# Kernel optimization log

Measured on AMD Instinct MI355X. Metric: run time of the kernel, lower is better.

## Reference

```python
import jax, jax.numpy as jnp
import numpy as np

G = 4      # deformable groups
K = 9      # 3x3 kernel points
EPS = 1e-5


def _bilinear_gather(value, loc_y, loc_x):
    # value: (N,H,W,G,Cg); loc_*: (N,H,W,G,K) float pixel coords, zero padding outside.
    N, H, W, g, Cg = value.shape
    y0f = jnp.floor(loc_y); x0f = jnp.floor(loc_x)
    wy = loc_y - y0f; wx = loc_x - x0f
    y0 = y0f.astype(jnp.int32); x0 = x0f.astype(jnp.int32)
    n_idx = jnp.arange(N).reshape(N, 1, 1, 1, 1)
    g_idx = jnp.arange(g).reshape(1, 1, 1, g, 1)

    def corner(yi, xi, w):
        valid = (yi >= 0) & (yi < H) & (xi >= 0) & (xi < W)
        yc = jnp.clip(yi, 0, H - 1); xc = jnp.clip(xi, 0, W - 1)
        v = value[n_idx, yc, xc, g_idx]  # (N,H,W,G,K,Cg) irregular gather
        return v * (w * valid)[..., None]

    return (corner(y0, x0, (1 - wy) * (1 - wx))
            + corner(y0, x0 + 1, (1 - wy) * wx)
            + corner(y0 + 1, x0, wy * (1 - wx))
            + corner(y0 + 1, x0 + 1, wy * wx))


def _dcnv4(t, H, W, Wv, bv, Wom, bom, Wo):
    # DCNv4 on (N,L,C): value proj -> learned-offset bilinear sampling with
    # UNNORMALIZED dynamic weights (no softmax, DCNv4) -> output proj (no bias).
    N, L, C = t.shape
    Cg = C // G
    value = (t @ Wv + bv).reshape(N, H, W, G, Cg)
    om = (t @ Wom + bom).reshape(N, H, W, G, 3 * K)
    offset = om[..., :2 * K].reshape(N, H, W, G, K, 2)  # (dx, dy) per point
    mask = om[..., 2 * K:]                               # (N,H,W,G,K)
    ky, kx = jnp.meshgrid(jnp.arange(-1, 2), jnp.arange(-1, 2), indexing='ij')
    ky = ky.reshape(-1).astype(t.dtype); kx = kx.reshape(-1).astype(t.dtype)
    ys = jnp.arange(H, dtype=t.dtype).reshape(1, H, 1, 1, 1)
    xs = jnp.arange(W, dtype=t.dtype).reshape(1, 1, W, 1, 1)
    loc_y = ys + ky + offset[..., 1]  # (N,H,W,G,K)
    loc_x = xs + kx + offset[..., 0]
    sampled = _bilinear_gather(value, loc_y, loc_x)  # (N,H,W,G,K,Cg)
    out = (sampled * mask[..., None]).sum(axis=4)    # (N,H,W,G,Cg)
    return out.reshape(N, L, C) @ Wo


def _bn(x, gamma, beta):
    # training-mode BatchNorm2d: per-channel batch stats over (N,H,W)
    mean = x.mean(axis=(0, 2, 3), keepdims=True)
    var = ((x - mean) ** 2).mean(axis=(0, 2, 3), keepdims=True)
    return (x - mean) * jax.lax.rsqrt(var + EPS) * gamma.reshape(1, -1, 1, 1) \
        + beta.reshape(1, -1, 1, 1)


def setup_inputs() -> dict:
    key = jax.random.key(0)
    ks = jax.random.split(key, 6)
    N, C, H, W = 4, 128, 64, 64
    s = 1.0 / np.sqrt(C)
    x = jax.random.normal(ks[0], (N, C, H, W), jnp.float32)
    Wv = jax.random.normal(ks[1], (C, C), jnp.float32) * s      # value_proj
    bv = jnp.zeros((C,), jnp.float32)
    Wom = jax.random.normal(ks[2], (C, G * 3 * K), jnp.float32) * 0.01  # offset+mask head
    bom = jnp.zeros((G * 3 * K,), jnp.float32)
    Wo = jax.random.normal(ks[3], (C, C), jnp.float32) * s      # output_proj (bias=False)
    gamma = jnp.ones((C,), jnp.float32)
    beta = jnp.zeros((C,), jnp.float32)
    Wc = jax.random.normal(ks[4], (C, C), jnp.float32) * s      # 1x1 conv (out=in=C)
    return {"x": x, "Wv": Wv, "bv": bv, "Wom": Wom, "bom": bom,
            "Wo": Wo, "gamma": gamma, "beta": beta, "Wc": Wc}


def reference(x, Wv, bv, Wom, bom, Wo, gamma, beta, Wc):
    N, C, H, W = x.shape
    shortcut = x
    t = x.transpose(0, 2, 3, 1).reshape(N, H * W, C)
    t = _dcnv4(t, H, W, Wv, bv, Wom, bom, Wo)
    y = t.reshape(N, H, W, C).transpose(0, 3, 1, 2)
    y = jax.nn.relu(_bn(y, gamma, beta))
    t = y.transpose(0, 2, 3, 1).reshape(N, H * W, C)
    t = _dcnv4(t, H, W, Wv, bv, Wom, bom, Wo)  # same DCNv4 weights reused
    y = t.reshape(N, H, W, C).transpose(0, 3, 1, 2)
    y = _bn(y, gamma, beta)                    # same BN params reused, no relu here
    y = y + shortcut                           # in_channels == out_channels
    return jnp.einsum('nchw,oc->nohw', y, Wc)  # final 1x1 conv
```

## Files before the change

### kernel.cpp

```cpp
#include <hip/hip_runtime.h>
#include <math.h>

#define CC   128
#define NL   16384
#define LHW  4096
#define OMP  112
#define HH   64
#define WW   64

typedef __attribute__((ext_vector_type(8))) short short8;
typedef __attribute__((ext_vector_type(4))) float f32x4;

__device__ __forceinline__ unsigned short f2bf(float f) {
    union { float f; unsigned u; } v; v.f = f;
    unsigned r = v.u + 0x7fff + ((v.u >> 16) & 1);
    return (unsigned short)(r >> 16);
}
__device__ __forceinline__ float bf2f(unsigned short u) {
    union { unsigned u; float f; } v; v.u = ((unsigned)u) << 16;
    return v.f;
}

__global__ __launch_bounds__(256) void prep_kernel(
    const float* __restrict__ Wv, const float* __restrict__ Wom,
    const float* __restrict__ Wo, const float* __restrict__ Wc,
    unsigned short* __restrict__ Wcomb, unsigned short* __restrict__ WoT,
    unsigned short* __restrict__ Wcb, float* __restrict__ stats)
{
    int tid = threadIdx.x;
    if (blockIdx.x == 0) {
        stats[tid] = 0.0f;
        stats[256 + tid] = 0.0f;
    }
    int i = blockIdx.x * 256 + tid;
    if (i < 16384) {
        int n = i >> 7, k = i & 127;
        Wcomb[i] = f2bf(Wv[k * CC + n]);
    } else if (i < 30720) {
        int j = i - 16384; int n = j >> 7, k = j & 127;
        Wcomb[16384 + j] = (n < 108) ? f2bf(Wom[k * 108 + n]) : (unsigned short)0;
    } else if (i < 47104) {
        int j = i - 30720; int n = j >> 7, k = j & 127;
        WoT[j] = f2bf(Wo[k * CC + n]);
    } else if (i < 63488) {
        int j = i - 47104;
        Wcb[j] = f2bf(Wc[j]);
    }
}

template<int IN_MODE>
__global__ __launch_bounds__(256) void gemm_vom_kernel(
    const float* __restrict__ Ain, const unsigned short* __restrict__ Wcomb,
    const float* __restrict__ bv, const float* __restrict__ bom,
    const float* __restrict__ stats, const float* __restrict__ gamma,
    const float* __restrict__ beta,
    unsigned short* __restrict__ val, float* __restrict__ omb)
{
    __shared__ unsigned short As[64 * 136];
    __shared__ unsigned short Bs[240 * 136];
    __shared__ float bnsc[128], bnsh[128];

    int tid = threadIdx.x;
    int block_m = blockIdx.x * 64;

    if (IN_MODE == 1 && tid < 128) {
        const float inv = 1.0f / 16384.0f;
        float mean = stats[tid] * inv;
        float var  = stats[128 + tid] * inv - mean * mean;
        float sc   = rsqrtf(var + 1e-5f) * gamma[tid];
        bnsc[tid] = sc;
        bnsh[tid] = beta[tid] - mean * sc;
    }

#pragma unroll
    for (int i = 0; i < 15; i++) {
        int id = tid + i * 256;
        int r = id >> 4, kc = id & 15;
        float4 v = *(const float4*)(Wcomb + (size_t)r * CC + kc * 8);
        *(float4*)(&Bs[r * 136 + kc * 8]) = v;
    }

    if (IN_MODE == 0) {
        int n   = block_m >> 12;
        int hw0 = block_m & 4095;
#pragma unroll
        for (int i = 0; i < 8; i++) {
            int id = tid + i * 256;
            int c  = id >> 4, j4 = id & 15;
            float4 v = *(const float4*)(Ain + (((size_t)(n * CC + c)) << 12) + hw0 + j4 * 4);
            As[(j4 * 4 + 0) * 136 + c] = f2bf(v.x);
            As[(j4 * 4 + 1) * 136 + c] = f2bf(v.y);
            As[(j4 * 4 + 2) * 136 + c] = f2bf(v.z);
            As[(j4 * 4 + 3) * 136 + c] = f2bf(v.w);
        }
    } else {
        __syncthreads();
#pragma unroll
        for (int i = 0; i < 8; i++) {
            int id = tid + i * 256;
            int r  = id >> 5, c4 = id & 31;
            float4 v = *(const float4*)(Ain + (size_t)(block_m + r) * CC + c4 * 4);
            int c = c4 * 4;
            float a0 = fmaxf(v.x * bnsc[c + 0] + bnsh[c + 0], 0.0f);
            float a1 = fmaxf(v.y * bnsc[c + 1] + bnsh[c + 1], 0.0f);
            float a2 = fmaxf(v.z * bnsc[c + 2] + bnsh[c + 2], 0.0f);
            float a3 = fmaxf(v.w * bnsc[c + 3] + bnsh[c + 3], 0.0f);
            As[r * 136 + c + 0] = f2bf(a0);
            As[r * 136 + c + 1] = f2bf(a1);
            As[r * 136 + c + 2] = f2bf(a2);
            As[r * 136 + c + 3] = f2bf(a3);
        }
    }
    __syncthreads();

    int w  = tid >> 6;
    int l  = tid & 63;
    int lr = l & 15, lk = l >> 4;

    f32x4 acc[15];
#pragma unroll
    for (int nt = 0; nt < 15; nt++) acc[nt] = (f32x4){0.f, 0.f, 0.f, 0.f};

#pragma unroll
    for (int kk = 0; kk < 4; kk++) {
        short8 a = *(const short8*)(&As[(w * 16 + lr) * 136 + kk * 32 + lk * 8]);
#pragma unroll
        for (int nt = 0; nt < 15; nt++) {
            short8 b = *(const short8*)(&Bs[(nt * 16 + lr) * 136 + kk * 32 + lk * 8]);
            acc[nt] = __builtin_amdgcn_mfma_f32_16x16x32_bf16(a, b, acc[nt], 0, 0, 0);
        }
    }

    int row0 = block_m + w * 16 + lk * 4;
#pragma unroll
    for (int nt = 0; nt < 8; nt++) {
        int col = nt * 16 + lr;
        float bb = bv[col];
#pragma unroll
        for (int r = 0; r < 4; r++)
            val[(size_t)(row0 + r) * CC + col] = f2bf(acc[nt][r] + bb);
    }
#pragma unroll
    for (int nt = 8; nt < 15; nt++) {
        int col = (nt - 8) * 16 + lr;
        float bb = (col < 108) ? bom[col] : 0.0f;
#pragma unroll
        for (int r = 0; r < 4; r++)
            omb[(size_t)(row0 + r) * OMP + col] = acc[nt][r] + bb;
    }
}

__global__ __launch_bounds__(256) void sample_kernel(
    const unsigned short* __restrict__ val, const float* __restrict__ omb,
    unsigned int* __restrict__ sbuf)
{
    int tid    = threadIdx.x;
    int gid    = blockIdx.x * 256 + tid;
    int unit   = gid >> 4;
    int lane16 = gid & 15;
    int nl = unit >> 2;
    int g  = unit & 3;
    int n  = nl >> 12;
    int hw = nl & 4095;
    int h  = hw >> 6;
    int w  = hw & 63;

    const float* omp = omb + (size_t)nl * OMP + g * 27;
    const unsigned short* vb = val + (((size_t)n) << 19) + g * 32 + lane16 * 2;

    float acc0 = 0.0f, acc1 = 0.0f;
#pragma unroll
    for (int k = 0; k < 9; k++) {
        float ox = omp[2 * k];
        float oy = omp[2 * k + 1];
        float mk = omp[18 + k];
        float ly = (float)(h + k / 3 - 1) + oy;
        float lx = (float)(w + k % 3 - 1) + ox;
        float y0f = floorf(ly), x0f = floorf(lx);
        float wy = ly - y0f, wx = lx - x0f;
        int y0 = (int)y0f, x0 = (int)x0f;

        float v0 = 0.0f, v1 = 0.0f;
#pragma unroll
        for (int cy = 0; cy < 2; cy++) {
#pragma unroll
            for (int cx = 0; cx < 2; cx++) {
                int yi = y0 + cy, xi = x0 + cx;
                float wgt = (cy ? wy : 1.0f - wy) * (cx ? wx : 1.0f - wx);
                bool valid = (yi >= 0) && (yi < HH) && (xi >= 0) && (xi < WW);
                wgt = valid ? wgt : 0.0f;
                int yc = min(max(yi, 0), HH - 1);
                int xc = min(max(xi, 0), WW - 1);
                unsigned int pv = *(const unsigned int*)(vb + (size_t)(yc * WW + xc) * CC);
                v0 += bf2f((unsigned short)(pv & 0xffff)) * wgt;
                v1 += bf2f((unsigned short)(pv >> 16)) * wgt;
            }
        }
        acc0 += mk * v0;
        acc1 += mk * v1;
    }
    unsigned int packed = (unsigned int)f2bf(acc0) | ((unsigned int)f2bf(acc1) << 16);
    sbuf[(size_t)nl * 64 + g * 16 + lane16] = packed;
}

__global__ __launch_bounds__(256) void gemm_o_bn_kernel(
    const unsigned short* __restrict__ A, const unsigned short* __restrict__ Bt,
    float* __restrict__ ybuf, float* __restrict__ stats)
{
    __shared__ unsigned short As[64 * 136];
    __shared__ unsigned short Bs[128 * 136];
    __shared__ float lstat[256];

    int tid = threadIdx.x;
    int block_m = blockIdx.x * 64;
    lstat[tid] = 0.0f;

#pragma unroll
    for (int i = 0; i < 4; i++) {
        int id = tid + i * 256;
        int r = id >> 4, kc = id & 15;
        float4 v = *(const float4*)(A + (size_t)(block_m + r) * CC + kc * 8);
        *(float4*)(&As[r * 136 + kc * 8]) = v;
    }
#pragma unroll
    for (int i = 0; i < 8; i++) {
        int id = tid + i * 256;
        int r = id >> 4, kc = id & 15;
        float4 v = *(const float4*)(Bt + (size_t)r * CC + kc * 8);
        *(float4*)(&Bs[r * 136 + kc * 8]) = v;
    }
    __syncthreads();

    int w  = tid >> 6;
    int l  = tid & 63;
    int wm = w & 1, wn = w >> 1;
    int lr = l & 15, lk = l >> 4;

    f32x4 acc[2][4];
#pragma unroll
    for (int mt = 0; mt < 2; mt++)
#pragma unroll
        for (int nt = 0; nt < 4; nt++) acc[mt][nt] = (f32x4){0.f, 0.f, 0.f, 0.f};

#pragma unroll
    for (int kk = 0; kk < 4; kk++) {
        short8 a[2], b[4];
#pragma unroll
        for (int mt = 0; mt < 2; mt++)
            a[mt] = *(const short8*)(&As[(wm * 32 + mt * 16 + lr) * 136 + kk * 32 + lk * 8]);
#pragma unroll
        for (int nt = 0; nt < 4; nt++)
            b[nt] = *(const short8*)(&Bs[(wn * 64 + nt * 16 + lr) * 136 + kk * 32 + lk * 8]);
#pragma unroll
        for (int mt = 0; mt < 2; mt++)
#pragma unroll
            for (int nt = 0; nt < 4; nt++)
                acc[mt][nt] = __builtin_amdgcn_mfma_f32_16x16x32_bf16(
                    a[mt], b[nt], acc[mt][nt], 0, 0, 0);
    }

#pragma unroll
    for (int nt = 0; nt < 4; nt++) {
        int col = wn * 64 + nt * 16 + lr;
        float s = 0.0f, sq = 0.0f;
#pragma unroll
        for (int mt = 0; mt < 2; mt++) {
            int row0 = block_m + wm * 32 + mt * 16 + lk * 4;
#pragma unroll
            for (int r = 0; r < 4; r++) {
                float v = acc[mt][nt][r];
                ybuf[(size_t)(row0 + r) * CC + col] = v;
                s += v;
                sq += v * v;
            }
        }
        atomicAdd(&lstat[col], s);
        atomicAdd(&lstat[128 + col], sq);
    }
    __syncthreads();
    if (tid < 128) {
        atomicAdd(&stats[tid], lstat[tid]);
        atomicAdd(&stats[128 + tid], lstat[128 + tid]);
    }
}

__global__ __launch_bounds__(256) void gemm_final_kernel(
    const float* __restrict__ ybuf, const float* __restrict__ x,
    const unsigned short* __restrict__ Bt, const float* __restrict__ stats,
    const float* __restrict__ gamma, const float* __restrict__ beta,
    float* __restrict__ out)
{
    __shared__ unsigned short As[64 * 136];
    __shared__ unsigned short Bs[128 * 136];
    __shared__ float Xs[64 * 132];
    __shared__ float bnsc[128], bnsh[128];

    int tid = threadIdx.x;
    int block_m = blockIdx.x * 64;
    int n   = block_m >> 12;
    int hw0 = block_m & 4095;

    if (tid < 128) {
        const float inv = 1.0f / 16384.0f;
        float mean = stats[tid] * inv;
        float var  = stats[128 + tid] * inv - mean * mean;
        float sc   = rsqrtf(var + 1e-5f) * gamma[tid];
        bnsc[tid] = sc;
        bnsh[tid] = beta[tid] - mean * sc;
    }

#pragma unroll
    for (int i = 0; i < 8; i++) {
        int id = tid + i * 256;
        int c  = id >> 4, j4 = id & 15;
        float4 v = *(const float4*)(x + (((size_t)(n * CC + c)) << 12) + hw0 + j4 * 4);
        Xs[(j4 * 4 + 0) * 132 + c] = v.x;
        Xs[(j4 * 4 + 1) * 132 + c] = v.y;
        Xs[(j4 * 4 + 2) * 132 + c] = v.z;
        Xs[(j4 * 4 + 3) * 132 + c] = v.w;
    }
#pragma unroll
    for (int i = 0; i < 8; i++) {
        int id = tid + i * 256;
        int r = id >> 4, kc = id & 15;
        float4 v = *(const float4*)(Bt + (size_t)r * CC + kc * 8);
        *(float4*)(&Bs[r * 136 + kc * 8]) = v;
    }
    __syncthreads();

#pragma unroll
    for (int i = 0; i < 8; i++) {
        int id = tid + i * 256;
        int r  = id >> 5, c4 = id & 31;
        float4 v = *(const float4*)(ybuf + (size_t)(block_m + r) * CC + c4 * 4);
        int c = c4 * 4;
        float a0 = v.x * bnsc[c + 0] + bnsh[c + 0] + Xs[r * 132 + c + 0];
        float a1 = v.y * bnsc[c + 1] + bnsh[c + 1] + Xs[r * 132 + c + 1];
        float a2 = v.z * bnsc[c + 2] + bnsh[c + 2] + Xs[r * 132 + c + 2];
        float a3 = v.w * bnsc[c + 3] + bnsh[c + 3] + Xs[r * 132 + c + 3];
        As[r * 136 + c + 0] = f2bf(a0);
        As[r * 136 + c + 1] = f2bf(a1);
        As[r * 136 + c + 2] = f2bf(a2);
        As[r * 136 + c + 3] = f2bf(a3);
    }
    __syncthreads();

    int w  = tid >> 6;
    int l  = tid & 63;
    int wm = w & 1, wn = w >> 1;
    int lr = l & 15, lk = l >> 4;

    f32x4 acc[2][4];
#pragma unroll
    for (int mt = 0; mt < 2; mt++)
#pragma unroll
        for (int nt = 0; nt < 4; nt++) acc[mt][nt] = (f32x4){0.f, 0.f, 0.f, 0.f};

#pragma unroll
    for (int kk = 0; kk < 4; kk++) {
        short8 a[2], b[4];
#pragma unroll
        for (int mt = 0; mt < 2; mt++)
            a[mt] = *(const short8*)(&As[(wm * 32 + mt * 16 + lr) * 136 + kk * 32 + lk * 8]);
#pragma unroll
        for (int nt = 0; nt < 4; nt++)
            b[nt] = *(const short8*)(&Bs[(wn * 64 + nt * 16 + lr) * 136 + kk * 32 + lk * 8]);
#pragma unroll
        for (int mt = 0; mt < 2; mt++)
#pragma unroll
            for (int nt = 0; nt < 4; nt++)
                acc[mt][nt] = __builtin_amdgcn_mfma_f32_16x16x32_bf16(
                    a[mt], b[nt], acc[mt][nt], 0, 0, 0);
    }

    __syncthreads();
    float* T = (float*)Bs;
#pragma unroll
    for (int mt = 0; mt < 2; mt++) {
        int rloc = wm * 32 + mt * 16 + lk * 4;
#pragma unroll
        for (int nt = 0; nt < 4; nt++) {
            int col = wn * 64 + nt * 16 + lr;
#pragma unroll
            for (int r = 0; r < 4; r++)
                T[col * 68 + rloc + r] = acc[mt][nt][r];
        }
    }
    __syncthreads();
    int o = tid >> 1, half = tid & 1;
    float* op = out + (((size_t)(n * CC + o)) << 12) + hw0 + half * 32;
#pragma unroll
    for (int i = 0; i < 8; i++) {
        float4 v = *(const float4*)(&T[o * 68 + half * 32 + i * 4]);
        *(float4*)(op + i * 4) = v;
    }
}

extern "C" void kernel_launch(void* const* d_in, const int* in_sizes, int n_in,
                              void* d_out, int out_size, void* d_ws, size_t ws_size,
                              hipStream_t stream)
{
    const float* x     = (const float*)d_in[0];
    const float* Wv    = (const float*)d_in[1];
    const float* bv    = (const float*)d_in[2];
    const float* Wom   = (const float*)d_in[3];
    const float* bom   = (const float*)d_in[4];
    const float* Wo    = (const float*)d_in[5];
    const float* gamma = (const float*)d_in[6];
    const float* beta  = (const float*)d_in[7];
    const float* Wc    = (const float*)d_in[8];
    float* out = (float*)d_out;

    char* ws = (char*)d_ws;
    unsigned short* val   = (unsigned short*)ws;   ws += (size_t)NL * CC * 2;
    float*          omb   = (float*)ws;            ws += (size_t)NL * OMP * 4;
    unsigned int*   sbuf  = (unsigned int*)ws;     ws += (size_t)NL * CC * 2;
    float*          ybuf  = (float*)ws;            ws += (size_t)NL * CC * 4;
    unsigned short* Wcomb = (unsigned short*)ws;   ws += 240 * 128 * 2;
    unsigned short* WoT   = (unsigned short*)ws;   ws += 128 * 128 * 2;
    unsigned short* Wcb   = (unsigned short*)ws;   ws += 128 * 128 * 2;
    float*          stats = (float*)ws;            ws += 2048;

    dim3 b256(256);

    prep_kernel<<<248, b256, 0, stream>>>(Wv, Wom, Wo, Wc, Wcomb, WoT, Wcb, stats);

    gemm_vom_kernel<0><<<256, b256, 0, stream>>>(x, Wcomb, bv, bom,
                                                 nullptr, nullptr, nullptr, val, omb);
    sample_kernel<<<4096, b256, 0, stream>>>(val, omb, sbuf);
    gemm_o_bn_kernel<<<256, b256, 0, stream>>>((const unsigned short*)sbuf, WoT, ybuf, stats);

    gemm_vom_kernel<1><<<256, b256, 0, stream>>>(ybuf, Wcomb, bv, bom,
                                                 stats, gamma, beta, val, omb);
    sample_kernel<<<4096, b256, 0, stream>>>(val, omb, sbuf);
    gemm_o_bn_kernel<<<256, b256, 0, stream>>>((const unsigned short*)sbuf, WoT, ybuf, stats + 256);

    gemm_final_kernel<<<256, b256, 0, stream>>>(ybuf, x, Wcb, stats + 256, gamma, beta, out);
}
```

Measured before the change: 156.7 us.

## Drop LDS staging in projection GEMMs, split per-wave tiles, pre-transpose input

New measurement: 180.3 us. 15.1% more time.

```diff
diff --git a/kernel.cpp b/kernel.cpp
--- a/kernel.cpp
+++ b/kernel.cpp
@@ -24,129 +24,153 @@
 __global__ __launch_bounds__(256) void prep_kernel(
     const float* __restrict__ Wv, const float* __restrict__ Wom,
     const float* __restrict__ Wo, const float* __restrict__ Wc,
+    const float* __restrict__ x,
     unsigned short* __restrict__ Wcomb, unsigned short* __restrict__ WoT,
-    unsigned short* __restrict__ Wcb, float* __restrict__ stats)
+    unsigned short* __restrict__ Wcb, unsigned short* __restrict__ xT,
+    float* __restrict__ stats)
 {
     int tid = threadIdx.x;
-    if (blockIdx.x == 0) {
-        stats[tid] = 0.0f;
-        stats[256 + tid] = 0.0f;
-    }
-    int i = blockIdx.x * 256 + tid;
-    if (i < 16384) {
-        int n = i >> 7, k = i & 127;
-        Wcomb[i] = f2bf(Wv[k * CC + n]);
-    } else if (i < 30720) {
-        int j = i - 16384; int n = j >> 7, k = j & 127;
-        Wcomb[16384 + j] = (n < 108) ? f2bf(Wom[k * 108 + n]) : (unsigned short)0;
-    } else if (i < 47104) {
-        int j = i - 30720; int n = j >> 7, k = j & 127;
-        WoT[j] = f2bf(Wo[k * CC + n]);
-    } else if (i < 63488) {
-        int j = i - 47104;
-        Wcb[j] = f2bf(Wc[j]);
+    int b = blockIdx.x;
+    if (b < 248) {
+        if (b == 0) {
+            stats[tid] = 0.0f;
+            stats[256 + tid] = 0.0f;
+        }
+        int i = b * 256 + tid;
+        if (i < 16384) {
+            int n = i >> 7, k = i & 127;
+            Wcomb[i] = f2bf(Wv[k * CC + n]);
+        } else if (i < 30720) {
+            int j = i - 16384; int n = j >> 7, k = j & 127;
+            Wcomb[16384 + j] = (n < 108) ? f2bf(Wom[k * 108 + n]) : (unsigned short)0;
+        } else if (i < 47104) {
+            int j = i - 30720; int n = j >> 7, k = j & 127;
+            WoT[j] = f2bf(Wo[k * CC + n]);
+        } else if (i < 63488) {
+            int j = i - 47104;
+            Wcb[j] = f2bf(Wc[j]);
+        }
+    } else {
+        __shared__ alignas(16) unsigned short As[64 * 136];
+        int block_m = (b - 248) * 64;
+        int n   = block_m >> 12;
+        int hw0 = block_m & 4095;
+#pragma unroll
+        for (int i = 0; i < 8; i++) {
+            int id = tid + i * 256;
+            int c  = id >> 4, j4 = id & 15;
+            float4 v = *(const float4*)(x + (((size_t)(n * CC + c)) << 12) + hw0 + j4 * 4);
+            As[(j4 * 4 + 0) * 136 + c] = f2bf(v.x);
+            As[(j4 * 4 + 1) * 136 + c] = f2bf(v.y);
+            As[(j4 * 4 + 2) * 136 + c] = f2bf(v.z);
+            As[(j4 * 4 + 3) * 136 + c] = f2bf(v.w);
+        }
+        __syncthreads();
+#pragma unroll
+        for (int i = 0; i < 4; i++) {
+            int id = tid + i * 256;
+            int r = id >> 4, kc = id & 15;
+            *(float4*)(xT + (size_t)(block_m + r) * CC + kc * 8) =
+                *(const float4*)(&As[r * 136 + kc * 8]);
+        }
     }
 }
 
 template<int IN_MODE>
-__global__ __launch_bounds__(256) void gemm_vom_kernel(
-    const float* __restrict__ Ain, const unsigned short* __restrict__ Wcomb,
+__global__ __launch_bounds__(256, 3) void gemm_vom_kernel(
+    const void* __restrict__ Ain_, const unsigned short* __restrict__ Wcomb,
     const float* __restrict__ bv, const float* __restrict__ bom,
     const float* __restrict__ stats, const float* __restrict__ gamma,
     const float* __restrict__ beta,
     unsigned short* __restrict__ val, float* __restrict__ omb)
 {
-    __shared__ unsigned short As[64 * 136];
-    __shared__ unsigned short Bs[240 * 136];
-    __shared__ float bnsc[128], bnsh[128];
+    __shared__ alignas(16) float bnsc[128];
+    __shared__ alignas(16) float bnsh[128];
 
     int tid = threadIdx.x;
-    int block_m = blockIdx.x * 64;
-
-    if (IN_MODE == 1 && tid < 128) {
-        const float inv = 1.0f / 16384.0f;
-        float mean = stats[tid] * inv;
-        float var  = stats[128 + tid] * inv - mean * mean;
-        float sc   = rsqrtf(var + 1e-5f) * gamma[tid];
-        bnsc[tid] = sc;
-        bnsh[tid] = beta[tid] - mean * sc;
-    }
-
-#pragma unroll
-    for (int i = 0; i < 15; i++) {
-        int id = tid + i * 256;
-        int r = id >> 4, kc = id & 15;
-        float4 v = *(const float4*)(Wcomb + (size_t)r * CC + kc * 8);
-        *(float4*)(&Bs[r * 136 + kc * 8]) = v;
-    }
-
-    if (IN_MODE == 0) {
-        int n   = block_m >> 12;
-        int hw0 = block_m & 4095;
-#pragma unroll
-        for (int i = 0; i < 8; i++) {
-            int id = tid + i * 256;
-            int c  = id >> 4, j4 = id & 15;
-            float4 v = *(const float4*)(Ain + (((size_t)(n * CC + c)) << 12) + hw0 + j4 * 4);
-            As[(j4 * 4 + 0) * 136 + c] = f2bf(v.x);
-            As[(j4 * 4 + 1) * 136 + c] = f2bf(v.y);
-            As[(j4 * 4 + 2) * 136 + c] = f2bf(v.z);
-            As[(j4 * 4 + 3) * 136 + c] = f2bf(v.w);
-        }
-    } else {
+    if (IN_MODE == 1) {
+        if (tid < 128) {
+            const float inv = 1.0f / 16384.0f;
+            float mean = stats[tid] * inv;
+            float var  = stats[128 + tid] * inv - mean * mean;
+            float sc   = rsqrtf(var + 1e-5f) * gamma[tid];
+            bnsc[tid] = sc;
+            bnsh[tid] = beta[tid] - mean * sc;
+        }
         __syncthreads();
-#pragma unroll
-        for (int i = 0; i < 8; i++) {
-            int id = tid + i * 256;
-            int r  = id >> 5, c4 = id & 31;
-            float4 v = *(const float4*)(Ain + (size_t)(block_m + r) * CC + c4 * 4);
-            int c = c4 * 4;
-            float a0 = fmaxf(v.x * bnsc[c + 0] + bnsh[c + 0], 0.0f);
-            float a1 = fmaxf(v.y * bnsc[c + 1] + bnsh[c + 1], 0.0f);
-            float a2 = fmaxf(v.z * bnsc[c + 2] + bnsh[c + 2], 0.0f);
-            float a3 = fmaxf(v.w * bnsc[c + 3] + bnsh[c + 3], 0.0f);
-            As[r * 136 + c + 0] = f2bf(a0);
-            As[r * 136 + c + 1] = f2bf(a1);
-            As[r * 136 + c + 2] = f2bf(a2);
-            As[r * 136 + c + 3] = f2bf(a3);
-        }
-    }
-    __syncthreads();
+    }
 
     int w  = tid >> 6;
     int l  = tid & 63;
     int lr = l & 15, lk = l >> 4;
 
-    f32x4 acc[15];
-#pragma unroll
-    for (int nt = 0; nt < 15; nt++) acc[nt] = (f32x4){0.f, 0.f, 0.f, 0.f};
-
-#pragma unroll
-    for (int kk = 0; kk < 4; kk++) {
-        short8 a = *(const short8*)(&As[(w * 16 + lr) * 136 + kk * 32 + lk * 8]);
-#pragma unroll
-        for (int nt = 0; nt < 15; nt++) {
-            short8 b = *(const short8*)(&Bs[(nt * 16 + lr) * 136 + kk * 32 + lk * 8]);
-            acc[nt] = __builtin_amdgcn_mfma_f32_16x16x32_bf16(a, b, acc[nt], 0, 0, 0);
-        }
-    }
-
-    int row0 = block_m + w * 16 + lk * 4;
-#pragma unroll
-    for (int nt = 0; nt < 8; nt++) {
-        int col = nt * 16 + lr;
-        float bb = bv[col];
-#pragma unroll
-        for (int r = 0; r < 4; r++)
-            val[(size_t)(row0 + r) * CC + col] = f2bf(acc[nt][r] + bb);
-    }
-#pragma unroll
-    for (int nt = 8; nt < 15; nt++) {
-        int col = (nt - 8) * 16 + lr;
-        float bb = (col < 108) ? bom[col] : 0.0f;
-#pragma unroll
-        for (int r = 0; r < 4; r++)
-            omb[(size_t)(row0 + r) * OMP + col] = acc[nt][r] + bb;
+    int wid = blockIdx.x * 4 + w;
+    int rt  = wid / 3;
+    int cc  = wid - rt * 3;
+    int row = rt * 16 + lr;
+
+    short8 a[4];
+    if (IN_MODE == 0) {
+        const unsigned short* ap = (const unsigned short*)Ain_ + (size_t)row * CC + lk * 8;
+#pragma unroll
+        for (int kk = 0; kk < 4; kk++)
+            a[kk] = *(const short8*)(ap + kk * 32);
+    } else {
+        const float* ap = (const float*)Ain_ + (size_t)row * CC + lk * 8;
+#pragma unroll
+        for (int kk = 0; kk < 4; kk++) {
+            float4 v0 = *(const float4*)(ap + kk * 32);
+            float4 v1 = *(const float4*)(ap + kk * 32 + 4);
+            int c = kk * 32 + lk * 8;
+            float4 s0 = *(const float4*)(&bnsc[c]);
+            float4 s1 = *(const float4*)(&bnsc[c + 4]);
+            float4 h0 = *(const float4*)(&bnsh[c]);
+            float4 h1 = *(const float4*)(&bnsh[c + 4]);
+            short8 t;
+            t[0] = (short)f2bf(fmaxf(v0.x * s0.x + h0.x, 0.0f));
+            t[1] = (short)f2bf(fmaxf(v0.y * s0.y + h0.y, 0.0f));
+            t[2] = (short)f2bf(fmaxf(v0.z * s0.z + h0.z, 0.0f));
+            t[3] = (short)f2bf(fmaxf(v0.w * s0.w + h0.w, 0.0f));
+            t[4] = (short)f2bf(fmaxf(v1.x * s1.x + h1.x, 0.0f));
+            t[5] = (short)f2bf(fmaxf(v1.y * s1.y + h1.y, 0.0f));
+            t[6] = (short)f2bf(fmaxf(v1.z * s1.z + h1.z, 0.0f));
+            t[7] = (short)f2bf(fmaxf(v1.w * s1.w + h1.w, 0.0f));
+            a[kk] = t;
+        }
+    }
+
+    int F = cc * 5;
+    f32x4 acc[5];
+#pragma unroll
+    for (int f = 0; f < 5; f++) acc[f] = (f32x4){0.f, 0.f, 0.f, 0.f};
+
+    const unsigned short* bp = Wcomb + (size_t)(F * 16 + lr) * CC + lk * 8;
+#pragma unroll
+    for (int f = 0; f < 5; f++) {
+#pragma unroll
+        for (int kk = 0; kk < 4; kk++) {
+            short8 bfr = *(const short8*)(bp + f * 16 * CC + kk * 32);
+            acc[f] = __builtin_amdgcn_mfma_f32_16x16x32_bf16(a[kk], bfr, acc[f], 0, 0, 0);
+        }
+    }
+
+    int row0 = rt * 16 + lk * 4;
+#pragma unroll
+    for (int f = 0; f < 5; f++) {
+        int frag = F + f;
+        if (frag < 8) {
+            int col = frag * 16 + lr;
+            float bb = bv[col];
+#pragma unroll
+            for (int r = 0; r < 4; r++)
+                val[(size_t)(row0 + r) * CC + col] = f2bf(acc[f][r] + bb);
+        } else {
+            int ocol = (frag - 8) * 16 + lr;
+            float bb = (ocol < 108) ? bom[ocol] : 0.0f;
+#pragma unroll
+            for (int r = 0; r < 4; r++)
+                omb[(size_t)(row0 + r) * OMP + ocol] = acc[f][r] + bb;
+        }
     }
 }
 
@@ -203,76 +227,56 @@
     sbuf[(size_t)nl * 64 + g * 16 + lane16] = packed;
 }
 
-__global__ __launch_bounds__(256) void gemm_o_bn_kernel(
+__global__ __launch_bounds__(512, 2) void gemm_o_bn_kernel(
     const unsigned short* __restrict__ A, const unsigned short* __restrict__ Bt,
     float* __restrict__ ybuf, float* __restrict__ stats)
 {
-    __shared__ unsigned short As[64 * 136];
-    __shared__ unsigned short Bs[128 * 136];
     __shared__ float lstat[256];
 
     int tid = threadIdx.x;
-    int block_m = blockIdx.x * 64;
-    lstat[tid] = 0.0f;
-
-#pragma unroll
-    for (int i = 0; i < 4; i++) {
-        int id = tid + i * 256;
-        int r = id >> 4, kc = id & 15;
-        float4 v = *(const float4*)(A + (size_t)(block_m + r) * CC + kc * 8);
-        *(float4*)(&As[r * 136 + kc * 8]) = v;
-    }
-#pragma unroll
-    for (int i = 0; i < 8; i++) {
-        int id = tid + i * 256;
-        int r = id >> 4, kc = id & 15;
-        float4 v = *(const float4*)(Bt + (size_t)r * CC + kc * 8);
-        *(float4*)(&Bs[r * 136 + kc * 8]) = v;
-    }
+    if (tid < 256) lstat[tid] = 0.0f;
     __syncthreads();
 
     int w  = tid >> 6;
     int l  = tid & 63;
-    int wm = w & 1, wn = w >> 1;
     int lr = l & 15, lk = l >> 4;
 
-    f32x4 acc[2][4];
-#pragma unroll
-    for (int mt = 0; mt < 2; mt++)
-#pragma unroll
-        for (int nt = 0; nt < 4; nt++) acc[mt][nt] = (f32x4){0.f, 0.f, 0.f, 0.f};
-
-#pragma unroll
-    for (int kk = 0; kk < 4; kk++) {
-        short8 a[2], b[4];
-#pragma unroll
-        for (int mt = 0; mt < 2; mt++)
-            a[mt] = *(const short8*)(&As[(wm * 32 + mt * 16 + lr) * 136 + kk * 32 + lk * 8]);
-#pragma unroll
-        for (int nt = 0; nt < 4; nt++)
-            b[nt] = *(const short8*)(&Bs[(wn * 64 + nt * 16 + lr) * 136 + kk * 32 + lk * 8]);
-#pragma unroll
-        for (int mt = 0; mt < 2; mt++)
-#pragma unroll
-            for (int nt = 0; nt < 4; nt++)
-                acc[mt][nt] = __builtin_amdgcn_mfma_f32_16x16x32_bf16(
-                    a[mt], b[nt], acc[mt][nt], 0, 0, 0);
-    }
-
-#pragma unroll
-    for (int nt = 0; nt < 4; nt++) {
-        int col = wn * 64 + nt * 16 + lr;
+    int wid = blockIdx.x * 8 + w;
+    int rt  = wid >> 1;
+    int cc  = wid & 1;
+    int row = rt * 16 + lr;
+
+    short8 a[4];
+    const unsigned short* ap = A + (size_t)row * CC + lk * 8;
+#pragma unroll
+    for (int kk = 0; kk < 4; kk++)
+        a[kk] = *(const short8*)(ap + kk * 32);
+
+    f32x4 acc[4];
+#pragma unroll
+    for (int f = 0; f < 4; f++) acc[f] = (f32x4){0.f, 0.f, 0.f, 0.f};
+
+    const unsigned short* bp = Bt + (size_t)(cc * 64 + lr) * CC + lk * 8;
+#pragma unroll
+    for (int f = 0; f < 4; f++) {
+#pragma unroll
+        for (int kk = 0; kk < 4; kk++) {
+            short8 bfr = *(const short8*)(bp + f * 16 * CC + kk * 32);
+            acc[f] = __builtin_amdgcn_mfma_f32_16x16x32_bf16(a[kk], bfr, acc[f], 0, 0, 0);
+        }
+    }
+
+    int row0 = rt * 16 + lk * 4;
+#pragma unroll
+    for (int f = 0; f < 4; f++) {
+        int col = cc * 64 + f * 16 + lr;
         float s = 0.0f, sq = 0.0f;
 #pragma unroll
-        for (int mt = 0; mt < 2; mt++) {
-            int row0 = block_m + wm * 32 + mt * 16 + lk * 4;
-#pragma unroll
-            for (int r = 0; r < 4; r++) {
-                float v = acc[mt][nt][r];
-                ybuf[(size_t)(row0 + r) * CC + col] = v;
-                s += v;
-                sq += v * v;
-            }
+        for (int r = 0; r < 4; r++) {
+            float v = acc[f][r];
+            ybuf[(size_t)(row0 + r) * CC + col] = v;
+            s += v;
+            sq += v * v;
         }
         atomicAdd(&lstat[col], s);
         atomicAdd(&lstat[128 + col], sq);
@@ -290,10 +294,11 @@
     const float* __restrict__ gamma, const float* __restrict__ beta,
     float* __restrict__ out)
 {
-    __shared__ unsigned short As[64 * 136];
-    __shared__ unsigned short Bs[128 * 136];
-    __shared__ float Xs[64 * 132];
-    __shared__ float bnsc[128], bnsh[128];
+    __shared__ alignas(16) unsigned short As[64 * 136];
+    __shared__ alignas(16) unsigned short Bs[128 * 136];
+    __shared__ alignas(16) float Xs[64 * 132];
+    __shared__ alignas(16) float bnsc[128];
+    __shared__ alignas(16) float bnsh[128];
 
     int tid = threadIdx.x;
     int block_m = blockIdx.x * 64;
@@ -420,20 +425,22 @@
     unsigned short* WoT   = (unsigned short*)ws;   ws += 128 * 128 * 2;
     unsigned short* Wcb   = (unsigned short*)ws;   ws += 128 * 128 * 2;
     float*          stats = (float*)ws;            ws += 2048;
+    unsigned short* xT    = (unsigned short*)ws;   ws += (size_t)NL * CC * 2;
 
     dim3 b256(256);
-
-    prep_kernel<<<248, b256, 0, stream>>>(Wv, Wom, Wo, Wc, Wcomb, WoT, Wcb, stats);
-
-    gemm_vom_kernel<0><<<256, b256, 0, stream>>>(x, Wcomb, bv, bom,
+    dim3 b512(512);
+
+    prep_kernel<<<504, b256, 0, stream>>>(Wv, Wom, Wo, Wc, x, Wcomb, WoT, Wcb, xT, stats);
+
+    gemm_vom_kernel<0><<<768, b256, 0, stream>>>(xT, Wcomb, bv, bom,
                                                  nullptr, nullptr, nullptr, val, omb);
     sample_kernel<<<4096, b256, 0, stream>>>(val, omb, sbuf);
-    gemm_o_bn_kernel<<<256, b256, 0, stream>>>((const unsigned short*)sbuf, WoT, ybuf, stats);
-
-    gemm_vom_kernel<1><<<256, b256, 0, stream>>>(ybuf, Wcomb, bv, bom,
+    gemm_o_bn_kernel<<<256, b512, 0, stream>>>((const unsigned short*)sbuf, WoT, ybuf, stats);
+
+    gemm_vom_kernel<1><<<768, b256, 0, stream>>>(ybuf, Wcomb, bv, bom,
                                                  stats, gamma, beta, val, omb);
     sample_kernel<<<4096, b256, 0, stream>>>(val, omb, sbuf);
-    gemm_o_bn_kernel<<<256, b256, 0, stream>>>((const unsigned short*)sbuf, WoT, ybuf, stats + 256);
+    gemm_o_bn_kernel<<<256, b512, 0, stream>>>((const unsigned short*)sbuf, WoT, ybuf, stats + 256);
 
     gemm_final_kernel<<<256, b256, 0, stream>>>(ybuf, x, Wcb, stats + 256, gamma, beta, out);
 }
```

## Fuse deformable sampling into output-projection GEMM and drop weight prep kernel

Applied to the files above, without the earlier changes.

Measured after the change: 173.1 us. +10.5%, slower.

```diff
diff --git a/kernel.cpp b/kernel.cpp
--- a/kernel.cpp
+++ b/kernel.cpp
@@ -3,7 +3,6 @@
 
 #define CC   128
 #define NL   16384
-#define LHW  4096
 #define OMP  112
 #define HH   64
 #define WW   64
@@ -21,63 +20,64 @@
     return v.f;
 }
 
-__global__ __launch_bounds__(256) void prep_kernel(
-    const float* __restrict__ Wv, const float* __restrict__ Wom,
-    const float* __restrict__ Wo, const float* __restrict__ Wc,
-    unsigned short* __restrict__ Wcomb, unsigned short* __restrict__ WoT,
-    unsigned short* __restrict__ Wcb, float* __restrict__ stats)
-{
-    int tid = threadIdx.x;
-    if (blockIdx.x == 0) {
-        stats[tid] = 0.0f;
-        stats[256 + tid] = 0.0f;
-    }
-    int i = blockIdx.x * 256 + tid;
-    if (i < 16384) {
-        int n = i >> 7, k = i & 127;
-        Wcomb[i] = f2bf(Wv[k * CC + n]);
-    } else if (i < 30720) {
-        int j = i - 16384; int n = j >> 7, k = j & 127;
-        Wcomb[16384 + j] = (n < 108) ? f2bf(Wom[k * 108 + n]) : (unsigned short)0;
-    } else if (i < 47104) {
-        int j = i - 30720; int n = j >> 7, k = j & 127;
-        WoT[j] = f2bf(Wo[k * CC + n]);
-    } else if (i < 63488) {
-        int j = i - 47104;
-        Wcb[j] = f2bf(Wc[j]);
-    }
-}
-
 template<int IN_MODE>
 __global__ __launch_bounds__(256) void gemm_vom_kernel(
-    const float* __restrict__ Ain, const unsigned short* __restrict__ Wcomb,
+    const float* __restrict__ Ain, const float* __restrict__ Wv,
+    const float* __restrict__ Wom,
     const float* __restrict__ bv, const float* __restrict__ bom,
-    const float* __restrict__ stats, const float* __restrict__ gamma,
-    const float* __restrict__ beta,
+    const float* __restrict__ stats_in, const float* __restrict__ gamma,
+    const float* __restrict__ beta, float* __restrict__ stats_zero,
     unsigned short* __restrict__ val, float* __restrict__ omb)
 {
-    __shared__ unsigned short As[64 * 136];
-    __shared__ unsigned short Bs[240 * 136];
+    __shared__ alignas(16) unsigned short As[64 * 136];
+    __shared__ alignas(16) unsigned short Bs[240 * 136];
     __shared__ float bnsc[128], bnsh[128];
 
     int tid = threadIdx.x;
     int block_m = blockIdx.x * 64;
 
-    if (IN_MODE == 1 && tid < 128) {
-        const float inv = 1.0f / 16384.0f;
-        float mean = stats[tid] * inv;
-        float var  = stats[128 + tid] * inv - mean * mean;
-        float sc   = rsqrtf(var + 1e-5f) * gamma[tid];
-        bnsc[tid] = sc;
-        bnsh[tid] = beta[tid] - mean * sc;
-    }
-
-#pragma unroll
-    for (int i = 0; i < 15; i++) {
+    if (IN_MODE == 0) {
+        if (blockIdx.x == 0) {
+            stats_zero[tid] = 0.0f;
+            stats_zero[256 + tid] = 0.0f;
+        }
+    } else {
+        if (tid < 128) {
+            const float inv = 1.0f / 16384.0f;
+            float mean = stats_in[tid] * inv;
+            float var  = stats_in[128 + tid] * inv - mean * mean;
+            float sc   = rsqrtf(var + 1e-5f) * gamma[tid];
+            bnsc[tid] = sc;
+            bnsh[tid] = beta[tid] - mean * sc;
+        }
+    }
+
+#pragma unroll
+    for (int i = 0; i < 16; i++) {
         int id = tid + i * 256;
-        int r = id >> 4, kc = id & 15;
-        float4 v = *(const float4*)(Wcomb + (size_t)r * CC + kc * 8);
-        *(float4*)(&Bs[r * 136 + kc * 8]) = v;
+        int k = id & 127, n4 = id >> 7;
+        float4 v = *(const float4*)(Wv + (size_t)k * CC + n4 * 4);
+        int nb0 = n4 * 4;
+        Bs[(nb0 + 0) * 136 + k] = f2bf(v.x);
+        Bs[(nb0 + 1) * 136 + k] = f2bf(v.y);
+        Bs[(nb0 + 2) * 136 + k] = f2bf(v.z);
+        Bs[(nb0 + 3) * 136 + k] = f2bf(v.w);
+    }
+#pragma unroll
+    for (int i = 0; i < 14; i++) {
+        int id = tid + i * 256;
+        int k = id & 127, n4 = id >> 7;
+        if (n4 < 27) {
+            float4 v = *(const float4*)(Wom + (size_t)k * 108 + n4 * 4);
+            int nb0 = 128 + n4 * 4;
+            Bs[(nb0 + 0) * 136 + k] = f2bf(v.x);
+            Bs[(nb0 + 1) * 136 + k] = f2bf(v.y);
+            Bs[(nb0 + 2) * 136 + k] = f2bf(v.z);
+            Bs[(nb0 + 3) * 136 + k] = f2bf(v.w);
+        } else {
+            Bs[236 * 136 + k] = 0; Bs[237 * 136 + k] = 0;
+            Bs[238 * 136 + k] = 0; Bs[239 * 136 + k] = 0;
+        }
     }
 
     if (IN_MODE == 0) {
@@ -150,129 +150,111 @@
     }
 }
 
-__global__ __launch_bounds__(256) void sample_kernel(
+__global__ __launch_bounds__(512, 4) void samp_obn_kernel(
     const unsigned short* __restrict__ val, const float* __restrict__ omb,
-    unsigned int* __restrict__ sbuf)
-{
-    int tid    = threadIdx.x;
-    int gid    = blockIdx.x * 256 + tid;
-    int unit   = gid >> 4;
-    int lane16 = gid & 15;
-    int nl = unit >> 2;
-    int g  = unit & 3;
-    int n  = nl >> 12;
-    int hw = nl & 4095;
-    int h  = hw >> 6;
-    int w  = hw & 63;
-
-    const float* omp = omb + (size_t)nl * OMP + g * 27;
-    const unsigned short* vb = val + (((size_t)n) << 19) + g * 32 + lane16 * 2;
-
-    float acc0 = 0.0f, acc1 = 0.0f;
-#pragma unroll
-    for (int k = 0; k < 9; k++) {
-        float ox = omp[2 * k];
-        float oy = omp[2 * k + 1];
-        float mk = omp[18 + k];
-        float ly = (float)(h + k / 3 - 1) + oy;
-        float lx = (float)(w + k % 3 - 1) + ox;
-        float y0f = floorf(ly), x0f = floorf(lx);
-        float wy = ly - y0f, wx = lx - x0f;
-        int y0 = (int)y0f, x0 = (int)x0f;
-
-        float v0 = 0.0f, v1 = 0.0f;
-#pragma unroll
-        for (int cy = 0; cy < 2; cy++) {
-#pragma unroll
-            for (int cx = 0; cx < 2; cx++) {
-                int yi = y0 + cy, xi = x0 + cx;
-                float wgt = (cy ? wy : 1.0f - wy) * (cx ? wx : 1.0f - wx);
-                bool valid = (yi >= 0) && (yi < HH) && (xi >= 0) && (xi < WW);
-                wgt = valid ? wgt : 0.0f;
-                int yc = min(max(yi, 0), HH - 1);
-                int xc = min(max(xi, 0), WW - 1);
-                unsigned int pv = *(const unsigned int*)(vb + (size_t)(yc * WW + xc) * CC);
-                v0 += bf2f((unsigned short)(pv & 0xffff)) * wgt;
-                v1 += bf2f((unsigned short)(pv >> 16)) * wgt;
-            }
-        }
-        acc0 += mk * v0;
-        acc1 += mk * v1;
-    }
-    unsigned int packed = (unsigned int)f2bf(acc0) | ((unsigned int)f2bf(acc1) << 16);
-    sbuf[(size_t)nl * 64 + g * 16 + lane16] = packed;
-}
-
-__global__ __launch_bounds__(256) void gemm_o_bn_kernel(
-    const unsigned short* __restrict__ A, const unsigned short* __restrict__ Bt,
+    const float* __restrict__ Wo,
     float* __restrict__ ybuf, float* __restrict__ stats)
 {
-    __shared__ unsigned short As[64 * 136];
-    __shared__ unsigned short Bs[128 * 136];
+    __shared__ alignas(16) unsigned short As[32 * 136];
+    __shared__ alignas(16) unsigned short Bs[128 * 136];
     __shared__ float lstat[256];
 
     int tid = threadIdx.x;
-    int block_m = blockIdx.x * 64;
-    lstat[tid] = 0.0f;
-
-#pragma unroll
+    int block_m = blockIdx.x * 32;
+    if (tid < 256) lstat[tid] = 0.0f;
+
+#pragma unroll
+    for (int i = 0; i < 8; i++) {
+        int id = tid + i * 512;
+        int k = id & 127, n4 = id >> 7;
+        float4 v = *(const float4*)(Wo + (size_t)k * CC + n4 * 4);
+        int nb0 = n4 * 4;
+        Bs[(nb0 + 0) * 136 + k] = f2bf(v.x);
+        Bs[(nb0 + 1) * 136 + k] = f2bf(v.y);
+        Bs[(nb0 + 2) * 136 + k] = f2bf(v.z);
+        Bs[(nb0 + 3) * 136 + k] = f2bf(v.w);
+    }
+
     for (int i = 0; i < 4; i++) {
-        int id = tid + i * 256;
-        int r = id >> 4, kc = id & 15;
-        float4 v = *(const float4*)(A + (size_t)(block_m + r) * CC + kc * 8);
-        *(float4*)(&As[r * 136 + kc * 8]) = v;
-    }
-#pragma unroll
-    for (int i = 0; i < 8; i++) {
-        int id = tid + i * 256;
-        int r = id >> 4, kc = id & 15;
-        float4 v = *(const float4*)(Bt + (size_t)r * CC + kc * 8);
-        *(float4*)(&Bs[r * 136 + kc * 8]) = v;
-    }
-    __syncthreads();
-
-    int w  = tid >> 6;
+        int t = tid + i * 512;
+        int lane16 = t & 15;
+        int ul = t >> 4;
+        int g  = ul & 3;
+        int rl = ul >> 2;
+        int nl = block_m + rl;
+        int n  = nl >> 12;
+        int hw = nl & 4095;
+        int h  = hw >> 6;
+        int w  = hw & 63;
+
+        const float* omp_ = omb + (size_t)nl * OMP + g * 27;
+        const unsigned short* vp = val + (((size_t)n) << 19) + g * 32 + lane16 * 2;
+
+        float acc0 = 0.0f, acc1 = 0.0f;
+#pragma unroll
+        for (int k = 0; k < 9; k++) {
+            float ox = omp_[2 * k];
+            float oy = omp_[2 * k + 1];
+            float mk = omp_[18 + k];
+            float ly = (float)(h + k / 3 - 1) + oy;
+            float lx = (float)(w + k % 3 - 1) + ox;
+            float y0f = floorf(ly), x0f = floorf(lx);
+            float wy = ly - y0f, wx = lx - x0f;
+            int y0 = (int)y0f, x0 = (int)x0f;
+
+            float v0 = 0.0f, v1 = 0.0f;
+#pragma unroll
+            for (int cy = 0; cy < 2; cy++) {
+#pragma unroll
+                for (int cx = 0; cx < 2; cx++) {
+                    int yi = y0 + cy, xi = x0 + cx;
+                    float wgt = (cy ? wy : 1.0f - wy) * (cx ? wx : 1.0f - wx);
+                    bool valid = (yi >= 0) && (yi < HH) && (xi >= 0) && (xi < WW);
+                    wgt = valid ? wgt : 0.0f;
+                    int yc = min(max(yi, 0), HH - 1);
+                    int xc = min(max(xi, 0), WW - 1);
+                    unsigned int pv = *(const unsigned int*)(vp + (size_t)(yc * WW + xc) * CC);
+                    v0 += bf2f((unsigned short)(pv & 0xffff)) * wgt;
+                    v1 += bf2f((unsigned short)(pv >> 16)) * wgt;
+                }
+            }
+            acc0 += mk * v0;
+            acc1 += mk * v1;
+        }
+        *(unsigned int*)(&As[rl * 136 + g * 32 + lane16 * 2]) =
+            (unsigned int)f2bf(acc0) | ((unsigned int)f2bf(acc1) << 16);
+    }
+    __syncthreads();
+
+    int w8 = tid >> 6;
     int l  = tid & 63;
-    int wm = w & 1, wn = w >> 1;
     int lr = l & 15, lk = l >> 4;
-
-    f32x4 acc[2][4];
-#pragma unroll
-    for (int mt = 0; mt < 2; mt++)
-#pragma unroll
-        for (int nt = 0; nt < 4; nt++) acc[mt][nt] = (f32x4){0.f, 0.f, 0.f, 0.f};
-
+    int wr = w8 & 1, wc = w8 >> 1;
+
+    f32x4 acc[2];
+    acc[0] = (f32x4){0.f, 0.f, 0.f, 0.f};
+    acc[1] = (f32x4){0.f, 0.f, 0.f, 0.f};
 #pragma unroll
     for (int kk = 0; kk < 4; kk++) {
-        short8 a[2], b[4];
-#pragma unroll
-        for (int mt = 0; mt < 2; mt++)
-            a[mt] = *(const short8*)(&As[(wm * 32 + mt * 16 + lr) * 136 + kk * 32 + lk * 8]);
-#pragma unroll
-        for (int nt = 0; nt < 4; nt++)
-            b[nt] = *(const short8*)(&Bs[(wn * 64 + nt * 16 + lr) * 136 + kk * 32 + lk * 8]);
-#pragma unroll
-        for (int mt = 0; mt < 2; mt++)
-#pragma unroll
-            for (int nt = 0; nt < 4; nt++)
-                acc[mt][nt] = __builtin_amdgcn_mfma_f32_16x16x32_bf16(
-                    a[mt], b[nt], acc[mt][nt], 0, 0, 0);
-    }
-
-#pragma unroll
-    for (int nt = 0; nt < 4; nt++) {
-        int col = wn * 64 + nt * 16 + lr;
+        short8 a = *(const short8*)(&As[(wr * 16 + lr) * 136 + kk * 32 + lk * 8]);
+#pragma unroll
+        for (int nt = 0; nt < 2; nt++) {
+            short8 b = *(const short8*)(&Bs[(wc * 32 + nt * 16 + lr) * 136 + kk * 32 + lk * 8]);
+            acc[nt] = __builtin_amdgcn_mfma_f32_16x16x32_bf16(a, b, acc[nt], 0, 0, 0);
+        }
+    }
+
+    int row0 = block_m + wr * 16 + lk * 4;
+#pragma unroll
+    for (int nt = 0; nt < 2; nt++) {
+        int col = wc * 32 + nt * 16 + lr;
         float s = 0.0f, sq = 0.0f;
 #pragma unroll
-        for (int mt = 0; mt < 2; mt++) {
-            int row0 = block_m + wm * 32 + mt * 16 + lk * 4;
-#pragma unroll
-            for (int r = 0; r < 4; r++) {
-                float v = acc[mt][nt][r];
-                ybuf[(size_t)(row0 + r) * CC + col] = v;
-                s += v;
-                sq += v * v;
-            }
+        for (int r = 0; r < 4; r++) {
+            float v = acc[nt][r];
+            ybuf[(size_t)(row0 + r) * CC + col] = v;
+            s += v;
+            sq += v * v;
         }
         atomicAdd(&lstat[col], s);
         atomicAdd(&lstat[128 + col], sq);
@@ -286,13 +268,13 @@
 
 __global__ __launch_bounds__(256) void gemm_final_kernel(
     const float* __restrict__ ybuf, const float* __restrict__ x,
-    const unsigned short* __restrict__ Bt, const float* __restrict__ stats,
+    const float* __restrict__ Wc, const float* __restrict__ stats,
     const float* __restrict__ gamma, const float* __restrict__ beta,
     float* __restrict__ out)
 {
-    __shared__ unsigned short As[64 * 136];
-    __shared__ unsigned short Bs[128 * 136];
-    __shared__ float Xs[64 * 132];
+    __shared__ alignas(16) unsigned short As[64 * 136];
+    __shared__ alignas(16) unsigned short Bs[128 * 136];
+    __shared__ alignas(16) float Xs[64 * 132];
     __shared__ float bnsc[128], bnsh[128];
 
     int tid = threadIdx.x;
@@ -320,11 +302,13 @@
         Xs[(j4 * 4 + 3) * 132 + c] = v.w;
     }
 #pragma unroll
-    for (int i = 0; i < 8; i++) {
+    for (int i = 0; i < 16; i++) {
         int id = tid + i * 256;
-        int r = id >> 4, kc = id & 15;
-        float4 v = *(const float4*)(Bt + (size_t)r * CC + kc * 8);
-        *(float4*)(&Bs[r * 136 + kc * 8]) = v;
+        int r = id >> 5, c4 = id & 31;
+        float4 v = *(const float4*)(Wc + (size_t)r * CC + c4 * 4);
+        unsigned short* p = &Bs[r * 136 + c4 * 4];
+        p[0] = f2bf(v.x); p[1] = f2bf(v.y);
+        p[2] = f2bf(v.z); p[3] = f2bf(v.w);
     }
     __syncthreads();
 
@@ -414,26 +398,20 @@
     char* ws = (char*)d_ws;
     unsigned short* val   = (unsigned short*)ws;   ws += (size_t)NL * CC * 2;
     float*          omb   = (float*)ws;            ws += (size_t)NL * OMP * 4;
-    unsigned int*   sbuf  = (unsigned int*)ws;     ws += (size_t)NL * CC * 2;
     float*          ybuf  = (float*)ws;            ws += (size_t)NL * CC * 4;
-    unsigned short* Wcomb = (unsigned short*)ws;   ws += 240 * 128 * 2;
-    unsigned short* WoT   = (unsigned short*)ws;   ws += 128 * 128 * 2;
-    unsigned short* Wcb   = (unsigned short*)ws;   ws += 128 * 128 * 2;
     float*          stats = (float*)ws;            ws += 2048;
 
-    dim3 b256(256);
-
-    prep_kernel<<<248, b256, 0, stream>>>(Wv, Wom, Wo, Wc, Wcomb, WoT, Wcb, stats);
-
-    gemm_vom_kernel<0><<<256, b256, 0, stream>>>(x, Wcomb, bv, bom,
-                                                 nullptr, nullptr, nullptr, val, omb);
-    sample_kernel<<<4096, b256, 0, stream>>>(val, omb, sbuf);
-    gemm_o_bn_kernel<<<256, b256, 0, stream>>>((const unsigned short*)sbuf, WoT, ybuf, stats);
-
-    gemm_vom_kernel<1><<<256, b256, 0, stream>>>(ybuf, Wcomb, bv, bom,
-                                                 stats, gamma, beta, val, omb);
-    sample_kernel<<<4096, b256, 0, stream>>>(val, omb, sbuf);
-    gemm_o_bn_kernel<<<256, b256, 0, stream>>>((const unsigned short*)sbuf, WoT, ybuf, stats + 256);
-
-    gemm_final_kernel<<<256, b256, 0, stream>>>(ybuf, x, Wcb, stats + 256, gamma, beta, out);
-}
+    dim3 b256(256), b512(512);
+
+    gemm_vom_kernel<0><<<256, b256, 0, stream>>>(x, Wv, Wom, bv, bom,
+                                                 nullptr, nullptr, nullptr,
+                                                 stats, val, omb);
+    samp_obn_kernel<<<512, b512, 0, stream>>>(val, omb, Wo, ybuf, stats);
+
+    gemm_vom_kernel<1><<<256, b256, 0, stream>>>(ybuf, Wv, Wom, bv, bom,
+                                                 stats, gamma, beta,
+                                                 nullptr, val, omb);
+    samp_obn_kernel<<<512, b512, 0, stream>>>(val, omb, Wo, ybuf, stats + 256);
+
+    gemm_final_kernel<<<256, b256, 0, stream>>>(ybuf, x, Wc, stats + 256, gamma, beta, out);
+}
```
